# Kernel tuning notes

Measured on AMD Instinct MI355X. Metric: run time of the kernel, lower is better.

## Reference

```python
import jax, jax.numpy as jnp
from jax import lax
import numpy as np
import math

B, W, C, H, K = 4, 1024, 1024, 16, 3  # batch, frames(cropsize), bins, num_bands, kernel
D = C // H  # head dim


def setup_inputs() -> dict:
    key = jax.random.key(0)
    ks = jax.random.split(key, 17)
    lin = lambda k: jax.random.normal(k, (C, C), jnp.float32) * 0.02
    vec = lambda k: jax.random.normal(k, (C,), jnp.float32) * 0.02
    cw = lambda k: jax.random.normal(k, (C, 1, K), jnp.float32) * 0.2  # depthwise conv weight (O, I/g=1, K)
    return {
        'x': jax.random.normal(ks[0], (B, W, C), jnp.float32),
        'qW': lin(ks[1]), 'qb': vec(ks[2]), 'qcw': cw(ks[3]), 'qcb': vec(ks[4]),
        'kW': lin(ks[5]), 'kb': vec(ks[6]), 'kcw': cw(ks[7]), 'kcb': vec(ks[8]),
        'vW': lin(ks[9]), 'vb': vec(ks[10]), 'vcw': cw(ks[11]), 'vcb': vec(ks[12]),
        'oW': lin(ks[13]), 'ob': vec(ks[14]),
        'er': jax.random.normal(ks[15], (D, W), jnp.float32),
    }


def _causal_dwconv(x_bwc, w, b):
    # x: (B, W, C) -> conv over time with left pad K-1, depthwise (groups=C)
    y = lax.conv_general_dilated(
        x_bwc.transpose(0, 2, 1), w, window_strides=(1,), padding=[(K - 1, 0)],
        feature_group_count=C, dimension_numbers=('NCH', 'OIH', 'NCH'))
    return (y + b[None, :, None]).transpose(0, 2, 1)


def reference(x, qW, qb, qcw, qcb, kW, kb, kcw, kcb, vW, vb, vcw, vcb, oW, ob, er):
    q = _causal_dwconv(x @ qW.T + qb, qcw, qcb).reshape(B, W, H, D).transpose(0, 2, 1, 3)  # bhwd
    k = _causal_dwconv(x @ kW.T + kb, kcw, kcb).reshape(B, W, H, D).transpose(0, 2, 3, 1)  # bhdw
    v = _causal_dwconv(x @ vW.T + vb, vcw, vcb).reshape(B, W, H, D).transpose(0, 2, 1, 3)  # bhwd
    # Music-Transformer relative position skewing
    p = jnp.pad(jnp.einsum('bhwd,dt->bhwt', q, er), ((0, 0), (0, 0), (0, 0), (1, 0)))
    p = p.transpose(0, 1, 3, 2)[:, :, 1:, :]  # (B,H,W,W)
    qk = (jnp.matmul(q, k) + p) / math.sqrt(C)
    a = jax.nn.softmax(qk, axis=-1)
    o = jnp.matmul(a, v).transpose(0, 2, 1, 3).reshape(B, W, C)
    return o @ oW.T + ob
```

## Files before the change

kernel.cpp:

```cpp
#include <hip/hip_runtime.h>

#define B_ 4
#define W_ 1024
#define C_ 1024
#define H_ 16
#define D_ 64

typedef __attribute__((ext_vector_type(8))) short short8;
typedef __attribute__((ext_vector_type(4))) float f32x4;

__device__ __forceinline__ unsigned short f2b(float f) {
  unsigned u = __builtin_bit_cast(unsigned, f);
  unsigned r = (u + 0x7fffu + ((u >> 16) & 1u)) >> 16;
  return (unsigned short)r;
}
__device__ __forceinline__ float b2f(short b) {
  return __builtin_bit_cast(float, ((unsigned)(unsigned short)b) << 16);
}
__device__ __forceinline__ unsigned pk2(float a, float b) {
  unsigned r;
  asm("v_cvt_pk_bf16_f32 %0, %1, %2" : "=v"(r) : "v"(a), "v"(b));
  return r;
}
__device__ __forceinline__ float ex2(float x) {
  float r;
  asm("v_exp_f32 %0, %1" : "=v"(r) : "v"(x));
  return r;
}

typedef __attribute__((address_space(1))) void GV;
typedef __attribute__((address_space(3))) void LV;
__device__ __forceinline__ void gl16(const short* g, short* l) {
  __builtin_amdgcn_global_load_lds((GV*)g, (LV*)l, 16, 0, 0);
}

__global__ __launch_bounds__(256)
void prep_kernel(const float* __restrict__ x, const float* __restrict__ qW,
                 const float* __restrict__ kW, const float* __restrict__ vW,
                 const float* __restrict__ oW, const float* __restrict__ er,
                 short* __restrict__ xh, short* __restrict__ wh,
                 short* __restrict__ ertb) {
  const int bx = blockIdx.x;
  const int tid = threadIdx.x;
  if (bx < 4096) {
    const float* s;
    short* d;
    size_t u;
    if (bx < 2048) {
      u = (size_t)bx * 256 + tid;
      s = x; d = xh;
    } else {
      u = (size_t)(bx - 2048) * 256 + tid;
      const int w = (int)(u >> 17);
      s = (w == 0) ? qW : (w == 1) ? kW : (w == 2) ? vW : oW;
      d = wh + (u & ~(size_t)131071) * 8;
      u &= 131071;
      const float4* p = (const float4*)s + u * 2;
      float4 a = p[0], b = p[1];
      short8 r;
      r[0] = f2b(a.x); r[1] = f2b(a.y); r[2] = f2b(a.z); r[3] = f2b(a.w);
      r[4] = f2b(b.x); r[5] = f2b(b.y); r[6] = f2b(b.z); r[7] = f2b(b.w);
      *((short8*)d + u) = r;
      return;
    }
    const float4* p = (const float4*)s + u * 2;
    float4 a = p[0], b = p[1];
    short8 r;
    r[0] = f2b(a.x); r[1] = f2b(a.y); r[2] = f2b(a.z); r[3] = f2b(a.w);
    r[4] = f2b(b.x); r[5] = f2b(b.y); r[6] = f2b(b.z); r[7] = f2b(b.w);
    *((short8*)d + u) = r;
  } else {
    int i = (bx - 4096) * 256 + tid;
    int d = i >> 8;
    int w4 = (i & 255) << 2;
    float4 v = *(const float4*)(er + (size_t)d * W_ + w4);
    ertb[(size_t)(w4 + 0) * D_ + d] = f2b(v.x);
    ertb[(size_t)(w4 + 1) * D_ + d] = f2b(v.y);
    ertb[(size_t)(w4 + 2) * D_ + d] = f2b(v.z);
    ertb[(size_t)(w4 + 3) * D_ + d] = f2b(v.w);
  }
}

#define GSTAGE(T, BUF)                                                       \
  {                                                                          \
    const int k0_ = (T) * 64;                                                \
    gl16(ga + (size_t)0  * K + k0_, sA[BUF] + 0    + ldst);                  \
    gl16(gb + (size_t)0  * K + k0_, sB[BUF] + 0    + ldst);                  \
    gl16(ga + (size_t)32 * K + k0_, sA[BUF] + 2048 + ldst);                  \
    gl16(gb + (size_t)32 * K + k0_, sB[BUF] + 2048 + ldst);                  \
    gl16(ga + (size_t)64 * K + k0_, sA[BUF] + 4096 + ldst);                  \
    gl16(gb + (size_t)64 * K + k0_, sB[BUF] + 4096 + ldst);                  \
    gl16(ga + (size_t)96 * K + k0_, sA[BUF] + 6144 + ldst);                  \
    gl16(gb + (size_t)96 * K + k0_, sB[BUF] + 6144 + ldst);                  \
  }

template <int OUTF32>
__global__ __launch_bounds__(256)
void gemm_bf16_v3(const short* __restrict__ A, const short* __restrict__ Wt,
                  const float* __restrict__ b0, const float* __restrict__ b1,
                  const float* __restrict__ b2, void* __restrict__ outv,
                  int M, int N, int K) {
  __shared__ short sA[2][128 * 64];
  __shared__ short sB[2][128 * 64];
  const int tid = threadIdx.x;
  const int bm = blockIdx.y * 128, bn = blockIdx.x * 128;
  const int wv = tid >> 6, lane = tid & 63;
  const int wr = (wv >> 1) * 64, wc = (wv & 1) * 64;
  const int l15 = lane & 15, l4 = lane >> 4;
  const int srow = tid >> 3;
  const int swsc = ((tid & 7) ^ (srow & 7)) * 8;
  const int cxor = (l15 & 7) * 8;
  const int ldst = tid * 8;
  const short* ga = A + (size_t)(bm + srow) * K + swsc;
  const short* gb = Wt + (size_t)(bn + srow) * K + swsc;

  f32x4 acc[4][4];
#pragma unroll
  for (int mf = 0; mf < 4; ++mf)
#pragma unroll
    for (int nf = 0; nf < 4; ++nf) acc[mf][nf] = (f32x4){0.f, 0.f, 0.f, 0.f};

  const int nt = K >> 6;
  GSTAGE(0, 0)
  for (int t = 0; t < nt; ++t) {
    const int cur = t & 1;
    if (t + 1 < nt) {
      GSTAGE(t + 1, cur ^ 1)
      asm volatile("s_waitcnt vmcnt(8)" ::: "memory");
    } else {
      asm volatile("s_waitcnt vmcnt(0)" ::: "memory");
    }
    __builtin_amdgcn_s_barrier();
    __builtin_amdgcn_sched_barrier(0);
#pragma unroll
    for (int ks = 0; ks < 2; ++ks) {
      short8 af[4], bf[4];
#pragma unroll
      for (int mf = 0; mf < 4; ++mf)
        af[mf] = *(short8*)(sA[cur] + (wr + mf * 16 + l15) * 64 + ((ks * 32 + l4 * 8) ^ cxor));
#pragma unroll
      for (int nf = 0; nf < 4; ++nf)
        bf[nf] = *(short8*)(sB[cur] + (wc + nf * 16 + l15) * 64 + ((ks * 32 + l4 * 8) ^ cxor));
#pragma unroll
      for (int mf = 0; mf < 4; ++mf)
#pragma unroll
        for (int nf = 0; nf < 4; ++nf)
          acc[mf][nf] = __builtin_amdgcn_mfma_f32_16x16x32_bf16(af[mf], bf[nf], acc[mf][nf], 0, 0, 0);
    }
    __builtin_amdgcn_sched_barrier(0);
    __builtin_amdgcn_s_barrier();
  }
#pragma unroll
  for (int mf = 0; mf < 4; ++mf) {
#pragma unroll
    for (int nf = 0; nf < 4; ++nf) {
      const int n = bn + wc + nf * 16 + l15;
      const float bs = (n < 1024) ? b0[n] : ((n < 2048) ? b1[n - 1024] : b2[n - 2048]);
#pragma unroll
      for (int r = 0; r < 4; ++r) {
        const int m = bm + wr + mf * 16 + l4 * 4 + r;
        const float v = acc[mf][nf][r] + bs;
        if (OUTF32) ((float*)outv)[(size_t)m * N + n] = v;
        else        ((short*)outv)[(size_t)m * N + n] = (short)f2b(v);
      }
    }
  }
}

__global__ __launch_bounds__(256)
void dwconv_qk_kernel(const short* __restrict__ yqkv,
                      const float* __restrict__ qcw, const float* __restrict__ qcb,
                      const float* __restrict__ kcw, const float* __restrict__ kcb,
                      short* __restrict__ qc, short* __restrict__ kc) {
  const int t = blockIdx.y;
  const float* cw = t ? kcw : qcw;
  const float* cb = t ? kcb : qcb;
  short* out = t ? kc : qc;
  const int idx = blockIdx.x * 256 + threadIdx.x;
  const int c8 = (idx & (C_ / 8 - 1)) << 3;
  const int bw = idx >> 7;
  const int w = bw & (W_ - 1);
  const short* base = yqkv + (size_t)bw * (3 * C_) + t * C_ + c8;
  short8 x2 = *(const short8*)base;
  short8 x1, x0;
  if (w >= 1) x1 = *(const short8*)(base - 3 * C_); else { for (int j = 0; j < 8; ++j) x1[j] = 0; }
  if (w >= 2) x0 = *(const short8*)(base - 6 * C_); else { for (int j = 0; j < 8; ++j) x0[j] = 0; }
  short8 r;
#pragma unroll
  for (int j = 0; j < 8; ++j) {
    const int c = c8 + j;
    float acc = b2f(x0[j]) * cw[c * 3 + 0] + b2f(x1[j]) * cw[c * 3 + 1] +
                b2f(x2[j]) * cw[c * 3 + 2] + cb[c];
    r[j] = (short)f2b(acc);
  }
  *(short8*)(out + (size_t)bw * C_ + c8) = r;
}

__global__ __launch_bounds__(256)
void dwconv_vt_kernel(const short* __restrict__ yqkv, const float* __restrict__ vcw,
                      const float* __restrict__ vcb, short* __restrict__ vt) {
  __shared__ short t[64][72];
  const int bh = blockIdx.y, w0 = blockIdx.x * 64;
  const int b = bh >> 4, h = bh & 15;
  const int tid = threadIdx.x;
  for (int c = tid; c < 512; c += 256) {
    const int w = c >> 3, dg = c & 7;
    const int gw = w0 + w;
    const short* base = yqkv + ((size_t)(b * W_ + gw)) * (3 * C_) + 2 * C_ + h * 64 + dg * 8;
    short8 x2 = *(const short8*)base;
    short8 x1, x0;
    if (gw >= 1) x1 = *(const short8*)(base - 3 * C_); else { for (int j = 0; j < 8; ++j) x1[j] = 0; }
    if (gw >= 2) x0 = *(const short8*)(base - 6 * C_); else { for (int j = 0; j < 8; ++j) x0[j] = 0; }
#pragma unroll
    for (int j = 0; j < 8; ++j) {
      const int ch = h * 64 + dg * 8 + j;
      float acc = b2f(x0[j]) * vcw[ch * 3 + 0] + b2f(x1[j]) * vcw[ch * 3 + 1] +
                  b2f(x2[j]) * vcw[ch * 3 + 2] + vcb[ch];
      t[dg * 8 + j][w] = (short)f2b(acc);
    }
  }
  __syncthreads();
  for (int c = tid; c < 512; c += 256) {
    const int d = c >> 3, wg = c & 7;
    *(short8*)(vt + ((size_t)(bh * 64 + d)) * W_ + w0 + wg * 8) = *(short8*)&t[d][wg * 8];
  }
}

__global__ __launch_bounds__(512, 4)
void attn_v4_kernel(const short* __restrict__ q, const short* __restrict__ k,
                    const short* __restrict__ vt, const short* __restrict__ ert,
                    short* __restrict__ o) {
  __shared__ short sK[2][4096];
  __shared__ short sQj[2][4096];
  __shared__ short sVt[2][4096];
  __shared__ short sP[128 * 64];

  const int tid = threadIdx.x;
  const int wid = blockIdx.x;
  const int swz = (wid & 7) * 64 + (wid >> 3);
  const int bh = swz >> 3, qt = swz & 7;
  const int b = bh >> 4, h = bh & 15;
  const int i0 = qt * 128;
  const int wv = tid >> 6, lane = tid & 63;
  const int l15 = lane & 15, l4 = lane >> 4;
  const size_t bW = (size_t)b * W_;
  const int srow = tid >> 3;
  const int swsc = ((tid & 7) ^ (srow & 7)) * 8;
  const int cxor = (l15 & 7) * 8;

  const short* qbase = q + bW * C_ + h * 64;
  const short* kbase = k + bW * C_ + h * 64;
  const short* vbase = vt + (size_t)bh * 64 * W_;

  gl16(kbase + (size_t)srow * C_ + swsc, sK[0] + tid * 8);
  gl16(qbase + (size_t)srow * C_ + swsc, sQj[0] + tid * 8);
  gl16(vbase + (size_t)srow * W_ + swsc, sVt[0] + tid * 8);

  short8 bQ[2], bE[2];
  {
    const int qi = i0 + wv * 16 + l15;
#pragma unroll
    for (int ks = 0; ks < 2; ++ks) {
      bQ[ks] = *(const short8*)(qbase + (size_t)qi * C_ + ks * 32 + l4 * 8);
      bE[ks] = *(const short8*)(ert + (size_t)qi * 64 + ks * 32 + l4 * 8);
    }
  }

  float m_ = -1e30f, l_ = 0.f;
  f32x4 accO[4];
#pragma unroll
  for (int mf = 0; mf < 4; ++mf) accO[mf] = (f32x4){0.f, 0.f, 0.f, 0.f};
  const float SC2 = 0.03125f * 1.44269504f;
  const float THR2 = 11.5416f;

  for (int jt = 0; jt < 16; ++jt) {
    const int cur = jt & 1;
    if (jt < 15) {
      const int j0n = (jt + 1) * 64;
      gl16(kbase + (size_t)(j0n + srow) * C_ + swsc, sK[cur ^ 1] + tid * 8);
      gl16(qbase + (size_t)(j0n + srow) * C_ + swsc, sQj[cur ^ 1] + tid * 8);
      gl16(vbase + (size_t)srow * W_ + j0n + swsc, sVt[cur ^ 1] + tid * 8);
      asm volatile("s_waitcnt vmcnt(3)" ::: "memory");
    } else {
      asm volatile("s_waitcnt vmcnt(0)" ::: "memory");
    }
    __builtin_amdgcn_s_barrier();
    __builtin_amdgcn_sched_barrier(0);

    f32x4 s[4];
#pragma unroll
    for (int mf = 0; mf < 4; ++mf) s[mf] = (f32x4){0.f, 0.f, 0.f, 0.f};
    const int ofA = (l4 * 8) ^ cxor;
    const int ofB = (32 + l4 * 8) ^ cxor;
    __builtin_amdgcn_s_setprio(1);
#pragma unroll
    for (int mf = 0; mf < 4; ++mf) {
      const short* kp = sK[cur] + (mf * 16 + l15) * 64;
      const short* jp = sQj[cur] + (mf * 16 + l15) * 64;
      s[mf] = __builtin_amdgcn_mfma_f32_16x16x32_bf16(*(short8*)(kp + ofA), bQ[0], s[mf], 0, 0, 0);
      s[mf] = __builtin_amdgcn_mfma_f32_16x16x32_bf16(*(short8*)(kp + ofB), bQ[1], s[mf], 0, 0, 0);
      s[mf] = __builtin_amdgcn_mfma_f32_16x16x32_bf16(*(short8*)(jp + ofA), bE[0], s[mf], 0, 0, 0);
      s[mf] = __builtin_amdgcn_mfma_f32_16x16x32_bf16(*(short8*)(jp + ofB), bE[1], s[mf], 0, 0, 0);
    }
    __builtin_amdgcn_s_setprio(0);

    float px = fmaxf(fmaxf(s[0][0], s[0][1]), fmaxf(s[0][2], s[0][3]));
#pragma unroll
    for (int mf = 1; mf < 4; ++mf)
      px = fmaxf(px, fmaxf(fmaxf(s[mf][0], s[mf][1]), fmaxf(s[mf][2], s[mf][3])));
    px = fmaxf(px, __shfl_xor(px, 16));
    px = fmaxf(px, __shfl_xor(px, 32));
    px *= SC2;
    if (!__all(px <= m_ + THR2)) {
      const float mn = fmaxf(m_, px);
      const float sc = ex2(m_ - mn);
      l_ *= sc;
#pragma unroll
      for (int mf = 0; mf < 4; ++mf)
#pragma unroll
        for (int r = 0; r < 4; ++r) accO[mf][r] *= sc;
      m_ = mn;
    }
    float p[4][4];
    float rs = 0.f;
#pragma unroll
    for (int mf = 0; mf < 4; ++mf)
#pragma unroll
      for (int r = 0; r < 4; ++r) {
        p[mf][r] = ex2(__builtin_fmaf(s[mf][r], SC2, -m_));
        rs += p[mf][r];
      }
    rs += __shfl_xor(rs, 16);
    rs += __shfl_xor(rs, 32);
    l_ += rs;

#pragma unroll
    for (int mf = 0; mf < 4; ++mf) {
      uint2 w2;
      w2.x = pk2(p[mf][0], p[mf][1]);
      w2.y = pk2(p[mf][2], p[mf][3]);
      const int off = (((2 * mf + (l4 >> 1)) ^ (l15 & 7)) * 8) + (l4 & 1) * 4;
      *(uint2*)(sP + (wv * 16 + l15) * 64 + off) = w2;
    }

    short8 pf[2];
#pragma unroll
    for (int ks = 0; ks < 2; ++ks)
      pf[ks] = *(short8*)(sP + (wv * 16 + l15) * 64 + ((ks * 32 + l4 * 8) ^ cxor));
    __builtin_amdgcn_s_setprio(1);
#pragma unroll
    for (int mf = 0; mf < 4; ++mf) {
      const short* vp = sVt[cur] + (mf * 16 + l15) * 64;
      accO[mf] = __builtin_amdgcn_mfma_f32_16x16x32_bf16(*(short8*)(vp + ofA), pf[0], accO[mf], 0, 0, 0);
      accO[mf] = __builtin_amdgcn_mfma_f32_16x16x32_bf16(*(short8*)(vp + ofB), pf[1], accO[mf], 0, 0, 0);
    }
    __builtin_amdgcn_s_setprio(0);

    __builtin_amdgcn_sched_barrier(0);
    __builtin_amdgcn_s_barrier();
  }

  const float inv = 1.f / l_;
  const size_t orow = (bW + i0 + wv * 16 + l15) * C_ + h * 64;
#pragma unroll
  for (int mf = 0; mf < 4; ++mf) {
    uint2 w2;
    w2.x = pk2(accO[mf][0] * inv, accO[mf][1] * inv);
    w2.y = pk2(accO[mf][2] * inv, accO[mf][3] * inv);
    *(uint2*)(o + orow + mf * 16 + l4 * 4) = w2;
  }
}

extern "C" void kernel_launch(void* const* d_in, const int* in_sizes, int n_in,
                              void* d_out, int out_size, void* d_ws, size_t ws_size,
                              hipStream_t stream) {
  (void)in_sizes; (void)n_in; (void)out_size; (void)ws_size;
  const float* x   = (const float*)d_in[0];
  const float* qW  = (const float*)d_in[1];
  const float* qb  = (const float*)d_in[2];
  const float* qcw = (const float*)d_in[3];
  const float* qcb = (const float*)d_in[4];
  const float* kW  = (const float*)d_in[5];
  const float* kb  = (const float*)d_in[6];
  const float* kcw = (const float*)d_in[7];
  const float* kcb = (const float*)d_in[8];
  const float* vW  = (const float*)d_in[9];
  const float* vb  = (const float*)d_in[10];
  const float* vcw = (const float*)d_in[11];
  const float* vcb = (const float*)d_in[12];
  const float* oW  = (const float*)d_in[13];
  const float* ob  = (const float*)d_in[14];
  const float* er  = (const float*)d_in[15];
  float* out = (float*)d_out;

  const size_t NE = (size_t)B_ * W_ * C_;
  const size_t NW = (size_t)C_ * C_;
  short* ws   = (short*)d_ws;
  short* xh    = ws;
  short* wqkvh = xh + NE;
  short* oWh   = wqkvh + 3 * NW;
  short* ertb  = oWh + NW;
  short* yqkv  = ertb + (size_t)W_ * D_;
  short* qc    = yqkv + (size_t)(B_ * W_) * (3 * C_);
  short* kc    = qc + NE;
  short* vt    = xh;
  short* oat   = yqkv;

  prep_kernel<<<4160, 256, 0, stream>>>(x, qW, kW, vW, oW, er, xh, wqkvh, ertb);

  const int M = B_ * W_;
  dim3 gq(3 * C_ / 128, M / 128);
  gemm_bf16_v3<0><<<gq, 256, 0, stream>>>(xh, wqkvh, qb, kb, vb, yqkv, M, 3 * C_, C_);

  dwconv_qk_kernel<<<dim3(2048, 2), 256, 0, stream>>>(yqkv, qcw, qcb, kcw, kcb, qc, kc);
  dwconv_vt_kernel<<<dim3(W_ / 64, B_ * H_), 256, 0, stream>>>(yqkv, vcw, vcb, vt);

  attn_v4_kernel<<<512, 512, 0, stream>>>(qc, kc, vt, ertb, oat);

  dim3 go(C_ / 128, M / 128);
  gemm_bf16_v3<1><<<go, 256, 0, stream>>>(oat, oWh, ob, ob, ob, out, M, C_, C_);
}
```

Measured before the change: 221.5 us.

## Halve GEMM K-tile to 32 with new swizzle and merge dwconv kernels

```diff
diff --git a/kernel.cpp b/kernel.cpp
--- a/kernel.cpp
+++ b/kernel.cpp
@@ -81,35 +81,31 @@
   }
 }
 
-#define GSTAGE(T, BUF)                                                       \
+#define GSTAGE32(T, BUF)                                                     \
   {                                                                          \
-    const int k0_ = (T) * 64;                                                \
-    gl16(ga + (size_t)0  * K + k0_, sA[BUF] + 0    + ldst);                  \
-    gl16(gb + (size_t)0  * K + k0_, sB[BUF] + 0    + ldst);                  \
-    gl16(ga + (size_t)32 * K + k0_, sA[BUF] + 2048 + ldst);                  \
-    gl16(gb + (size_t)32 * K + k0_, sB[BUF] + 2048 + ldst);                  \
-    gl16(ga + (size_t)64 * K + k0_, sA[BUF] + 4096 + ldst);                  \
-    gl16(gb + (size_t)64 * K + k0_, sB[BUF] + 4096 + ldst);                  \
-    gl16(ga + (size_t)96 * K + k0_, sA[BUF] + 6144 + ldst);                  \
-    gl16(gb + (size_t)96 * K + k0_, sB[BUF] + 6144 + ldst);                  \
+    const int k0_ = (T) * 32;                                                \
+    gl16(ga + (size_t)0  * K + k0_, sA[BUF] + ldst);                         \
+    gl16(gb + (size_t)0  * K + k0_, sB[BUF] + ldst);                         \
+    gl16(ga + (size_t)64 * K + k0_, sA[BUF] + 2048 + ldst);                  \
+    gl16(gb + (size_t)64 * K + k0_, sB[BUF] + 2048 + ldst);                  \
   }
 
 template <int OUTF32>
 __global__ __launch_bounds__(256)
-void gemm_bf16_v3(const short* __restrict__ A, const short* __restrict__ Wt,
+void gemm_bf16_v4(const short* __restrict__ A, const short* __restrict__ Wt,
                   const float* __restrict__ b0, const float* __restrict__ b1,
                   const float* __restrict__ b2, void* __restrict__ outv,
                   int M, int N, int K) {
-  __shared__ short sA[2][128 * 64];
-  __shared__ short sB[2][128 * 64];
+  __shared__ short sA[2][128 * 32];
+  __shared__ short sB[2][128 * 32];
   const int tid = threadIdx.x;
   const int bm = blockIdx.y * 128, bn = blockIdx.x * 128;
   const int wv = tid >> 6, lane = tid & 63;
   const int wr = (wv >> 1) * 64, wc = (wv & 1) * 64;
   const int l15 = lane & 15, l4 = lane >> 4;
-  const int srow = tid >> 3;
-  const int swsc = ((tid & 7) ^ (srow & 7)) * 8;
-  const int cxor = (l15 & 7) * 8;
+  const int srow = tid >> 2;
+  const int swsc = ((tid & 3) ^ ((srow >> 1) & 3)) * 8;
+  const int rxor = ((l15 >> 1) & 3) * 8;
   const int ldst = tid * 8;
   const short* ga = A + (size_t)(bm + srow) * K + swsc;
   const short* gb = Wt + (size_t)(bn + srow) * K + swsc;
@@ -120,33 +116,30 @@
 #pragma unroll
     for (int nf = 0; nf < 4; ++nf) acc[mf][nf] = (f32x4){0.f, 0.f, 0.f, 0.f};
 
-  const int nt = K >> 6;
-  GSTAGE(0, 0)
+  const int nt = K >> 5;
+  GSTAGE32(0, 0)
   for (int t = 0; t < nt; ++t) {
     const int cur = t & 1;
     if (t + 1 < nt) {
-      GSTAGE(t + 1, cur ^ 1)
-      asm volatile("s_waitcnt vmcnt(8)" ::: "memory");
+      GSTAGE32(t + 1, cur ^ 1)
+      asm volatile("s_waitcnt vmcnt(4)" ::: "memory");
     } else {
       asm volatile("s_waitcnt vmcnt(0)" ::: "memory");
     }
     __builtin_amdgcn_s_barrier();
     __builtin_amdgcn_sched_barrier(0);
-#pragma unroll
-    for (int ks = 0; ks < 2; ++ks) {
-      short8 af[4], bf[4];
-#pragma unroll
-      for (int mf = 0; mf < 4; ++mf)
-        af[mf] = *(short8*)(sA[cur] + (wr + mf * 16 + l15) * 64 + ((ks * 32 + l4 * 8) ^ cxor));
+    short8 af[4], bf[4];
+#pragma unroll
+    for (int mf = 0; mf < 4; ++mf)
+      af[mf] = *(short8*)(sA[cur] + (wr + mf * 16 + l15) * 32 + ((l4 * 8) ^ rxor));
+#pragma unroll
+    for (int nf = 0; nf < 4; ++nf)
+      bf[nf] = *(short8*)(sB[cur] + (wc + nf * 16 + l15) * 32 + ((l4 * 8) ^ rxor));
+#pragma unroll
+    for (int mf = 0; mf < 4; ++mf)
 #pragma unroll
       for (int nf = 0; nf < 4; ++nf)
-        bf[nf] = *(short8*)(sB[cur] + (wc + nf * 16 + l15) * 64 + ((ks * 32 + l4 * 8) ^ cxor));
-#pragma unroll
-      for (int mf = 0; mf < 4; ++mf)
-#pragma unroll
-        for (int nf = 0; nf < 4; ++nf)
-          acc[mf][nf] = __builtin_amdgcn_mfma_f32_16x16x32_bf16(af[mf], bf[nf], acc[mf][nf], 0, 0, 0);
-    }
+        acc[mf][nf] = __builtin_amdgcn_mfma_f32_16x16x32_bf16(af[mf], bf[nf], acc[mf][nf], 0, 0, 0);
     __builtin_amdgcn_sched_barrier(0);
     __builtin_amdgcn_s_barrier();
   }
@@ -168,61 +161,63 @@
 }
 
 __global__ __launch_bounds__(256)
-void dwconv_qk_kernel(const short* __restrict__ yqkv,
-                      const float* __restrict__ qcw, const float* __restrict__ qcb,
-                      const float* __restrict__ kcw, const float* __restrict__ kcb,
-                      short* __restrict__ qc, short* __restrict__ kc) {
-  const int t = blockIdx.y;
-  const float* cw = t ? kcw : qcw;
-  const float* cb = t ? kcb : qcb;
-  short* out = t ? kc : qc;
-  const int idx = blockIdx.x * 256 + threadIdx.x;
-  const int c8 = (idx & (C_ / 8 - 1)) << 3;
-  const int bw = idx >> 7;
-  const int w = bw & (W_ - 1);
-  const short* base = yqkv + (size_t)bw * (3 * C_) + t * C_ + c8;
-  short8 x2 = *(const short8*)base;
-  short8 x1, x0;
-  if (w >= 1) x1 = *(const short8*)(base - 3 * C_); else { for (int j = 0; j < 8; ++j) x1[j] = 0; }
-  if (w >= 2) x0 = *(const short8*)(base - 6 * C_); else { for (int j = 0; j < 8; ++j) x0[j] = 0; }
-  short8 r;
-#pragma unroll
-  for (int j = 0; j < 8; ++j) {
-    const int c = c8 + j;
-    float acc = b2f(x0[j]) * cw[c * 3 + 0] + b2f(x1[j]) * cw[c * 3 + 1] +
-                b2f(x2[j]) * cw[c * 3 + 2] + cb[c];
-    r[j] = (short)f2b(acc);
-  }
-  *(short8*)(out + (size_t)bw * C_ + c8) = r;
-}
-
-__global__ __launch_bounds__(256)
-void dwconv_vt_kernel(const short* __restrict__ yqkv, const float* __restrict__ vcw,
-                      const float* __restrict__ vcb, short* __restrict__ vt) {
-  __shared__ short t[64][72];
-  const int bh = blockIdx.y, w0 = blockIdx.x * 64;
-  const int b = bh >> 4, h = bh & 15;
+void dwconv_all_kernel(const short* __restrict__ yqkv,
+                       const float* __restrict__ qcw, const float* __restrict__ qcb,
+                       const float* __restrict__ kcw, const float* __restrict__ kcb,
+                       const float* __restrict__ vcw, const float* __restrict__ vcb,
+                       short* __restrict__ qc, short* __restrict__ kc,
+                       short* __restrict__ vt) {
+  __shared__ short t_[64][72];
+  const int bx = blockIdx.x;
   const int tid = threadIdx.x;
-  for (int c = tid; c < 512; c += 256) {
-    const int w = c >> 3, dg = c & 7;
-    const int gw = w0 + w;
-    const short* base = yqkv + ((size_t)(b * W_ + gw)) * (3 * C_) + 2 * C_ + h * 64 + dg * 8;
+  if (bx < 4096) {
+    const int t = bx >> 11;
+    const float* cw = t ? kcw : qcw;
+    const float* cb = t ? kcb : qcb;
+    short* out = t ? kc : qc;
+    const int idx = (bx & 2047) * 256 + tid;
+    const int c8 = (idx & (C_ / 8 - 1)) << 3;
+    const int bw = idx >> 7;
+    const int w = bw & (W_ - 1);
+    const short* base = yqkv + (size_t)bw * (3 * C_) + t * C_ + c8;
     short8 x2 = *(const short8*)base;
     short8 x1, x0;
-    if (gw >= 1) x1 = *(const short8*)(base - 3 * C_); else { for (int j = 0; j < 8; ++j) x1[j] = 0; }
-    if (gw >= 2) x0 = *(const short8*)(base - 6 * C_); else { for (int j = 0; j < 8; ++j) x0[j] = 0; }
+    if (w >= 1) x1 = *(const short8*)(base - 3 * C_); else { for (int j = 0; j < 8; ++j) x1[j] = 0; }
+    if (w >= 2) x0 = *(const short8*)(base - 6 * C_); else { for (int j = 0; j < 8; ++j) x0[j] = 0; }
+    short8 r;
 #pragma unroll
     for (int j = 0; j < 8; ++j) {
-      const int ch = h * 64 + dg * 8 + j;
-      float acc = b2f(x0[j]) * vcw[ch * 3 + 0] + b2f(x1[j]) * vcw[ch * 3 + 1] +
-                  b2f(x2[j]) * vcw[ch * 3 + 2] + vcb[ch];
-      t[dg * 8 + j][w] = (short)f2b(acc);
-    }
-  }
-  __syncthreads();
-  for (int c = tid; c < 512; c += 256) {
-    const int d = c >> 3, wg = c & 7;
-    *(short8*)(vt + ((size_t)(bh * 64 + d)) * W_ + w0 + wg * 8) = *(short8*)&t[d][wg * 8];
+      const int c = c8 + j;
+      float acc = b2f(x0[j]) * cw[c * 3 + 0] + b2f(x1[j]) * cw[c * 3 + 1] +
+                  b2f(x2[j]) * cw[c * 3 + 2] + cb[c];
+      r[j] = (short)f2b(acc);
+    }
+    *(short8*)(out + (size_t)bw * C_ + c8) = r;
+  } else {
+    const int bx2 = bx - 4096;
+    const int w0 = (bx2 & 15) * 64, bh = bx2 >> 4;
+    const int b = bh >> 4, h = bh & 15;
+    for (int c = tid; c < 512; c += 256) {
+      const int w = c >> 3, dg = c & 7;
+      const int gw = w0 + w;
+      const short* base = yqkv + ((size_t)(b * W_ + gw)) * (3 * C_) + 2 * C_ + h * 64 + dg * 8;
+      short8 x2 = *(const short8*)base;
+      short8 x1, x0;
+      if (gw >= 1) x1 = *(const short8*)(base - 3 * C_); else { for (int j = 0; j < 8; ++j) x1[j] = 0; }
+      if (gw >= 2) x0 = *(const short8*)(base - 6 * C_); else { for (int j = 0; j < 8; ++j) x0[j] = 0; }
+#pragma unroll
+      for (int j = 0; j < 8; ++j) {
+        const int ch = h * 64 + dg * 8 + j;
+        float acc = b2f(x0[j]) * vcw[ch * 3 + 0] + b2f(x1[j]) * vcw[ch * 3 + 1] +
+                    b2f(x2[j]) * vcw[ch * 3 + 2] + vcb[ch];
+        t_[dg * 8 + j][w] = (short)f2b(acc);
+      }
+    }
+    __syncthreads();
+    for (int c = tid; c < 512; c += 256) {
+      const int d = c >> 3, wg = c & 7;
+      *(short8*)(vt + ((size_t)(bh * 64 + d)) * W_ + w0 + wg * 8) = *(short8*)&t_[d][wg * 8];
+    }
   }
 }
 
@@ -410,13 +405,13 @@
 
   const int M = B_ * W_;
   dim3 gq(3 * C_ / 128, M / 128);
-  gemm_bf16_v3<0><<<gq, 256, 0, stream>>>(xh, wqkvh, qb, kb, vb, yqkv, M, 3 * C_, C_);
-
-  dwconv_qk_kernel<<<dim3(2048, 2), 256, 0, stream>>>(yqkv, qcw, qcb, kcw, kcb, qc, kc);
-  dwconv_vt_kernel<<<dim3(W_ / 64, B_ * H_), 256, 0, stream>>>(yqkv, vcw, vcb, vt);
+  gemm_bf16_v4<0><<<gq, 256, 0, stream>>>(xh, wqkvh, qb, kb, vb, yqkv, M, 3 * C_, C_);
+
+  dwconv_all_kernel<<<5120, 256, 0, stream>>>(yqkv, qcw, qcb, kcw, kcb, vcw, vcb,
+                                              qc, kc, vt);
 
   attn_v4_kernel<<<512, 512, 0, stream>>>(qc, kc, vt, ertb, oat);
 
   dim3 go(C_ / 128, M / 128);
-  gemm_bf16_v3<1><<<go, 256, 0, stream>>>(oat, oWh, ob, ob, ob, out, M, C_, C_);
-}
+  gemm_bf16_v4<1><<<go, 256, 0, stream>>>(oat, oWh, ob, ob, ob, out, M, C_, C_);
+}
```

Result: faster. 215.6 us (-2.7%).
